# Performance work log

Measured on AMD Instinct MI355X. Metric: run time of the kernel, lower is better.

The kernel has to match this reference:

```python
import jax, jax.numpy as jnp
import numpy as np

B, N, K, C = 8, 8192, 16, 64
POS_HID, MULT = 64, 4
BN_EPS = 1e-3  # keras BatchNormalization default


def _bn(x, gamma, beta):
    # inference-mode BN with init moving stats (mean=0, var=1)
    return gamma * x * (1.0 / np.sqrt(1.0 + BN_EPS)) + beta


def setup_inputs() -> dict:
    key = jax.random.key(0)
    ks = jax.random.split(key, 16)
    d = {
        "key": jax.random.normal(ks[0], (B, N, C), jnp.float32),
        "query": jax.random.normal(ks[1], (B, N, C), jnp.float32),
        "value": jax.random.normal(ks[2], (B, N, C), jnp.float32),
        "pos": jax.random.normal(ks[3], (B, N, 3), jnp.float32),
        "idx": jax.random.randint(ks[4], (B, N, K), 0, N, jnp.int32),
        # pos_conv1: 1x1 conv 3 -> POS_HID (glorot), + BN params
        "W1": jax.random.normal(ks[5], (3, POS_HID), jnp.float32) * np.sqrt(2.0 / (3 + POS_HID)),
        "b1": jnp.zeros((POS_HID,), jnp.float32),
        "g1": jnp.ones((POS_HID,), jnp.float32) + 0.1 * jax.random.normal(ks[6], (POS_HID,), jnp.float32),
        "bt1": 0.1 * jax.random.normal(ks[7], (POS_HID,), jnp.float32),
        # pos_conv2: POS_HID -> C, no activation
        "W2": jax.random.normal(ks[8], (POS_HID, C), jnp.float32) * np.sqrt(2.0 / (POS_HID + C)),
        "b2": jnp.zeros((C,), jnp.float32),
        # attn_mlp1: C -> MULT*C, BN + relu
        "W3": jax.random.normal(ks[9], (C, MULT * C), jnp.float32) * np.sqrt(2.0 / (C + MULT * C)),
        "b3": jnp.zeros((MULT * C,), jnp.float32),
        "g3": jnp.ones((MULT * C,), jnp.float32) + 0.1 * jax.random.normal(ks[10], (MULT * C,), jnp.float32),
        "bt3": 0.1 * jax.random.normal(ks[11], (MULT * C,), jnp.float32),
        # attn_mlp2: MULT*C -> C, no activation
        "W4": jax.random.normal(ks[12], (MULT * C, C), jnp.float32) * np.sqrt(2.0 / (MULT * C + C)),
        "b4": jnp.zeros((C,), jnp.float32),
    }
    return d


def reference(key, query, value, pos, idx, W1, b1, g1, bt1, W2, b2, W3, b3, g3, bt3, W4, b4):
    # per-batch KNN gather: key [B,N,C], idx [B,N,K] -> [B,N,K,C]
    gather = jax.vmap(lambda t, i: t[i])
    k_nb = gather(key, idx)                         # [B,N,K,C]
    qk_rel = query[:, :, None, :] - k_nb            # [B,N,K,C]
    pos_rel = pos[:, :, None, :] - gather(pos, idx)  # [B,N,K,3]

    # positional embedding MLP (1x1 convs)
    h = jax.nn.relu(_bn(pos_rel @ W1 + b1, g1, bt1))  # [B,N,K,POS_HID]
    pos_em = h @ W2 + b2                              # [B,N,K,C]

    # attention MLP (subtraction-based vector attention)
    a = jax.nn.relu(_bn((qk_rel + pos_em) @ W3 + b3, g3, bt3))  # [B,N,K,4C]
    a = (a @ W4 + b4) / jnp.sqrt(jnp.asarray(C, jnp.float32))   # [B,N,K,C]
    # tf.nn.softmax default axis=-1 -> softmax over CHANNEL axis (faithful to source)
    a = jax.nn.softmax(a, axis=-1)

    v = value[:, :, None, :] + pos_em               # [B,N,K,C]
    # einsum 'b c i j, b c i j -> b c j' on channels-last: sum over neighbor axis K
    agg = jnp.sum(a * v, axis=2)                    # [B,N,C]
    return agg
```

## Files before the change

### kernel.cpp

```cpp
#include <hip/hip_runtime.h>
#include <hip/hip_bf16.h>

typedef __bf16 bf16x8 __attribute__((ext_vector_type(8)));
typedef __bf16 bf16x4 __attribute__((ext_vector_type(4)));
typedef float  f32x4  __attribute__((ext_vector_type(4)));

#define MFMA16(A,B,C) __builtin_amdgcn_mfma_f32_16x16x32_bf16((A),(B),(C),0,0,0)

constexpr int NB = 8, NN = 8192, KK = 16;
constexpr int XS = 72;
constexpr size_t WS_NEEDED = 78848;


__global__ void prep_kernel(const float* __restrict__ W1, const float* __restrict__ b1,
                            const float* __restrict__ g1, const float* __restrict__ bt1,
                            const float* __restrict__ W2, const float* __restrict__ W3,
                            const float* __restrict__ b3, const float* __restrict__ g3,
                            const float* __restrict__ bt3, const float* __restrict__ W4,
                            unsigned char* __restrict__ ws)
{
    __bf16* w3f = (__bf16*)(ws);
    __bf16* w4f = (__bf16*)(ws + 32768);
    __bf16* w2f = (__bf16*)(ws + 65536);
    __bf16* w1f = (__bf16*)(ws + 73728);
    float*  c3f = (float*)(ws + 77824);

    const float inv = 1.0f / sqrtf(1.0f + 1e-3f);
    int t = blockIdx.x * 256 + threadIdx.x;

    if (t < 16384) {
        int i = t & 7, lane = (t >> 3) & 63, r = t >> 9;
        int ks = r & 1, nb = r >> 1;
        int p = ks * 32 + (lane >> 4) * 8 + i;
        int c = (p & 3) * 16 + (p >> 2);
        int n = nb * 16 + (lane & 15);
        w3f[t] = (__bf16)(W3[c * 256 + n] * (g3[n] * inv));
    } else if (t < 32768) {
        int u = t - 16384;
        int i = u & 7, lane = (u >> 3) & 63, r = u >> 9;
        int kb = r & 7, nb = r >> 3;
        int q = (kb & 1) * 32 + (lane >> 4) * 8 + i;
        int c = (kb >> 1) * 64 + (q & 3) * 16 + (q >> 2);
        int n = nb * 16 + (lane & 15);
        w4f[u] = (__bf16)(W4[c * 64 + n] * 0.125f);
    } else if (t < 36864) {
        int u = t - 32768;
        int i = u & 7, lane = (u >> 3) & 63, r = u >> 9;
        int ks = r & 1, nb = r >> 1;
        int p = ks * 32 + (lane >> 4) * 8 + i;
        int c = (p & 3) * 16 + (p >> 2);
        int n = nb * 16 + (lane & 15);
        w2f[u] = (__bf16)(W2[c * 64 + n]);
    } else if (t < 38912) {
        int u = t - 36864;
        int i = u & 7, lane = (u >> 3) & 63, nb = u >> 9;
        int kk = (lane >> 4) * 8 + i;
        int n = nb * 16 + (lane & 15);
        float v = 0.f;
        if (kk < 3)       v = W1[kk * 64 + n] * (g1[n] * inv);
        else if (kk == 3) v = b1[n] * (g1[n] * inv) + bt1[n];
        w1f[u] = (__bf16)v;
    } else if (t < 39168) {
        int n = t - 38912;
        c3f[n] = b3[n] * (g3[n] * inv) + bt3[n];
    }
}

__global__ __launch_bounds__(256, 2) void fused_kernel(
    const float* __restrict__ key, const float* __restrict__ query,
    const float* __restrict__ value, const float* __restrict__ pos,
    const int* __restrict__ idx, const float* __restrict__ b2,
    const float* __restrict__ b4, const unsigned char* __restrict__ ws,
    float* __restrict__ out)
{
    const __bf16* w3f = (const __bf16*)(ws);
    const __bf16* w4f = (const __bf16*)(ws + 32768);
    const __bf16* w2f = (const __bf16*)(ws + 65536);
    const __bf16* w1f = (const __bf16*)(ws + 73728);
    const float*  c3f = (const float*)(ws + 77824);

    const f32x4 ZERO4 = {0.f, 0.f, 0.f, 0.f};

    __shared__ __attribute__((aligned(16))) __bf16 sX [4][32 * XS];
    __shared__ __attribute__((aligned(16))) __bf16 sA1[4][32 * XS];
    __shared__ __attribute__((aligned(16))) float  sPR[4][32][4];
    __shared__ int sJ[4][32];

    const int wv   = threadIdx.x >> 6;
    const int lane = threadIdx.x & 63;
    const int lg   = lane >> 4;
    const int ln   = lane & 15;

    const int ptbase = blockIdx.x * 8 + wv * 2;
    const int b  = ptbase >> 13;
    const int n0 = ptbase & 8191;

    __bf16* X  = sX[wv];
    __bf16* A1 = sA1[wv];

    if (lane < 32) {
        int p = lane >> 4, k = lane & 15;
        int n = n0 + p;
        int j = idx[(b * NN + n) * KK + k];
        sJ[wv][lane] = j;
        int pb = (b * NN + n) * 3, jb = (b * NN + j) * 3;
        sPR[wv][lane][0] = pos[pb + 0] - pos[jb + 0];
        sPR[wv][lane][1] = pos[pb + 1] - pos[jb + 1];
        sPR[wv][lane][2] = pos[pb + 2] - pos[jb + 2];
        sPR[wv][lane][3] = 0.f;
    }
    bf16x8 af[2];
    #pragma unroll
    for (int rb = 0; rb < 2; ++rb) {
        bf16x8 a;
        #pragma unroll
        for (int i = 0; i < 8; ++i) a[i] = (__bf16)0.0f;
        if (lg == 0) {
            const float4 pr = *(const float4*)&sPR[wv][rb * 16 + ln][0];
            a[0] = (__bf16)pr.x; a[1] = (__bf16)pr.y; a[2] = (__bf16)pr.z;
            a[3] = (__bf16)1.0f;
        }
        af[rb] = a;
    }
    f32x4 pa[2][4];
    #pragma unroll
    for (int nb = 0; nb < 4; ++nb) {
        bf16x8 wf = *(const bf16x8*)(w1f + (size_t)(nb * 64 + lane) * 8);
        pa[0][nb] = MFMA16(af[0], wf, ZERO4);
        pa[1][nb] = MFMA16(af[1], wf, ZERO4);
    }
    #pragma unroll
    for (int rb = 0; rb < 2; ++rb)
        #pragma unroll
        for (int jj = 0; jj < 4; ++jj) {
            int row = rb * 16 + lg * 4 + jj;
            bf16x4 hv;
            #pragma unroll
            for (int nb = 0; nb < 4; ++nb) hv[nb] = (__bf16)fmaxf(pa[rb][nb][jj], 0.f);
            *(bf16x4*)&X[row * XS + ln * 4] = hv;
        }

    bf16x8 hf[2][2];
    #pragma unroll
    for (int rb = 0; rb < 2; ++rb)
        #pragma unroll
        for (int ks = 0; ks < 2; ++ks)
            hf[rb][ks] = *(const bf16x8*)&X[(rb * 16 + ln) * XS + ks * 32 + lg * 8];
    f32x4 pacc[2][4];
    #pragma unroll
    for (int rb = 0; rb < 2; ++rb)
        #pragma unroll
        for (int cb = 0; cb < 4; ++cb) pacc[rb][cb] = ZERO4;
    #pragma unroll
    for (int cb = 0; cb < 4; ++cb)
        #pragma unroll
        for (int ks = 0; ks < 2; ++ks) {
            bf16x8 wf = *(const bf16x8*)(w2f + (size_t)((cb * 2 + ks) * 64 + lane) * 8);
            pacc[0][cb] = MFMA16(hf[0][ks], wf, pacc[0][cb]);
            pacc[1][cb] = MFMA16(hf[1][ks], wf, pacc[1][cb]);
        }

    float posem[2][4][4];
    #pragma unroll
    for (int rb = 0; rb < 2; ++rb) {
        const int nrow = n0 + rb;
        float qv[4];
        #pragma unroll
        for (int cb = 0; cb < 4; ++cb) {
            qv[cb] = query[(b * NN + nrow) * 64 + cb * 16 + ln];
            float c2v = b2[cb * 16 + ln];
            #pragma unroll
            for (int jj = 0; jj < 4; ++jj)
                posem[rb][cb][jj] = pacc[rb][cb][jj] + c2v;
        }
        #pragma unroll
        for (int jj = 0; jj < 4; ++jj) {
            int row = rb * 16 + lg * 4 + jj;
            int jb = (b * NN + sJ[wv][row]) * 64;
            bf16x4 xv;
            #pragma unroll
            for (int cb = 0; cb < 4; ++cb)
                xv[cb] = (__bf16)(qv[cb] - key[jb + cb * 16 + ln] + posem[rb][cb][jj]);
            *(bf16x4*)&X[row * XS + ln * 4] = xv;
        }
    }

    bf16x8 xf[2][2];
    #pragma unroll
    for (int rb = 0; rb < 2; ++rb)
        #pragma unroll
        for (int ks = 0; ks < 2; ++ks)
            xf[rb][ks] = *(const bf16x8*)&X[(rb * 16 + ln) * XS + ks * 32 + lg * 8];
    f32x4 acc2[2][4];
    #pragma unroll
    for (int rb = 0; rb < 2; ++rb)
        #pragma unroll
        for (int nb = 0; nb < 4; ++nb) acc2[rb][nb] = ZERO4;

    for (int cc = 0; cc < 4; ++cc) {
        f32x4 g1a[2][4];
        #pragma unroll
        for (int rb = 0; rb < 2; ++rb)
            #pragma unroll
            for (int cb = 0; cb < 4; ++cb) g1a[rb][cb] = ZERO4;
        #pragma unroll
        for (int cb = 0; cb < 4; ++cb) {
            int nb = cc * 4 + cb;
            #pragma unroll
            for (int ks = 0; ks < 2; ++ks) {
                bf16x8 wf = *(const bf16x8*)(w3f + (size_t)((nb * 2 + ks) * 64 + lane) * 8);
                g1a[0][cb] = MFMA16(xf[0][ks], wf, g1a[0][cb]);
                g1a[1][cb] = MFMA16(xf[1][ks], wf, g1a[1][cb]);
            }
        }
        float c3v[4];
        #pragma unroll
        for (int cb = 0; cb < 4; ++cb) c3v[cb] = c3f[(cc * 4 + cb) * 16 + ln];
        #pragma unroll
        for (int rb = 0; rb < 2; ++rb)
            #pragma unroll
            for (int jj = 0; jj < 4; ++jj) {
                int row = rb * 16 + lg * 4 + jj;
                bf16x4 av;
                #pragma unroll
                for (int cb = 0; cb < 4; ++cb)
                    av[cb] = (__bf16)fmaxf(g1a[rb][cb][jj] + c3v[cb], 0.f);
                *(bf16x4*)&A1[row * XS + ln * 4] = av;
            }
        #pragma unroll
        for (int kb2 = 0; kb2 < 2; ++kb2) {
            bf16x8 a1f[2];
            #pragma unroll
            for (int rb = 0; rb < 2; ++rb)
                a1f[rb] = *(const bf16x8*)&A1[(rb * 16 + ln) * XS + kb2 * 32 + lg * 8];
            #pragma unroll
            for (int nb = 0; nb < 4; ++nb) {
                bf16x8 wf = *(const bf16x8*)(w4f + (size_t)((nb * 8 + cc * 2 + kb2) * 64 + lane) * 8);
                acc2[0][nb] = MFMA16(a1f[0], wf, acc2[0][nb]);
                acc2[1][nb] = MFMA16(a1f[1], wf, acc2[1][nb]);
            }
        }
    }

    float b4v[4];
    #pragma unroll
    for (int nb = 0; nb < 4; ++nb) b4v[nb] = b4[nb * 16 + ln] * 0.125f;
    #pragma unroll
    for (int rb = 0; rb < 2; ++rb) {
        const int nrow = n0 + rb;
        float vv[4];
        #pragma unroll
        for (int nb = 0; nb < 4; ++nb) vv[nb] = value[(b * NN + nrow) * 64 + nb * 16 + ln];

        float res[4] = {0.f, 0.f, 0.f, 0.f};
        #pragma unroll
        for (int jj = 0; jj < 4; ++jj) {
            float e0 = __expf(acc2[rb][0][jj] + b4v[0]);
            float e1 = __expf(acc2[rb][1][jj] + b4v[1]);
            float e2 = __expf(acc2[rb][2][jj] + b4v[2]);
            float e3 = __expf(acc2[rb][3][jj] + b4v[3]);
            float s = (e0 + e1) + (e2 + e3);
            #pragma unroll
            for (int d = 1; d < 16; d <<= 1) s += __shfl_xor(s, d, 64);
            float inv = 1.0f / s;
            res[0] = fmaf(e0 * inv, vv[0] + posem[rb][0][jj], res[0]);
            res[1] = fmaf(e1 * inv, vv[1] + posem[rb][1][jj], res[1]);
            res[2] = fmaf(e2 * inv, vv[2] + posem[rb][2][jj], res[2]);
            res[3] = fmaf(e3 * inv, vv[3] + posem[rb][3][jj], res[3]);
        }
        #pragma unroll
        for (int nb = 0; nb < 4; ++nb) {
            res[nb] += __shfl_xor(res[nb], 16, 64);
            res[nb] += __shfl_xor(res[nb], 32, 64);
        }
        float o = (lg == 0) ? res[0] : (lg == 1) ? res[1] : (lg == 2) ? res[2] : res[3];
        out[(b * NN + nrow) * 64 + lane] = o;
    }
}

extern "C" void kernel_launch(void* const* d_in, const int* in_sizes, int n_in,
                              void* d_out, int out_size, void* d_ws, size_t ws_size,
                              hipStream_t stream) {
    const float* key   = (const float*)d_in[0];
    const float* query = (const float*)d_in[1];
    const float* value = (const float*)d_in[2];
    const float* pos   = (const float*)d_in[3];
    const int*   idx   = (const int*)d_in[4];
    const float* W1    = (const float*)d_in[5];
    const float* b1    = (const float*)d_in[6];
    const float* g1    = (const float*)d_in[7];
    const float* bt1   = (const float*)d_in[8];
    const float* W2    = (const float*)d_in[9];
    const float* b2    = (const float*)d_in[10];
    const float* W3    = (const float*)d_in[11];
    const float* b3    = (const float*)d_in[12];
    const float* g3    = (const float*)d_in[13];
    const float* bt3   = (const float*)d_in[14];
    const float* W4    = (const float*)d_in[15];
    const float* b4    = (const float*)d_in[16];
    unsigned char* ws  = (unsigned char*)d_ws;
    float* out = (float*)d_out;

    if (ws_size < WS_NEEDED) return;

    hipLaunchKernelGGL(prep_kernel, dim3(153), dim3(256), 0, stream,
                       W1, b1, g1, bt1, W2, W3, b3, g3, bt3, W4, ws);
    hipLaunchKernelGGL(fused_kernel, dim3(8192), dim3(256), 0, stream,
                       key, query, value, pos, idx, b2, b4, ws, out);
}
```

Before: 262.0 us.

## Hoist global loads early and fold biases into MFMA accumulator init

Moves the query, value, bias and gathered key loads to the start of the kernel so their latency overlaps the positional MLP MFMAs. Neighbour indices and relative positions now stay in registers and are broadcast with shuffles instead of going through shared memory. The b2, c3 and b4 biases are preloaded into the MFMA accumulators, which removes the separate add passes. The cost is more live registers, which at launch bounds (256,2) could cause spills or lower occupancy.

```diff
diff --git a/kernel.cpp b/kernel.cpp
--- a/kernel.cpp
+++ b/kernel.cpp
@@ -83,8 +83,6 @@
 
     __shared__ __attribute__((aligned(16))) __bf16 sX [4][32 * XS];
     __shared__ __attribute__((aligned(16))) __bf16 sA1[4][32 * XS];
-    __shared__ __attribute__((aligned(16))) float  sPR[4][32][4];
-    __shared__ int sJ[4][32];
 
     const int wv   = threadIdx.x >> 6;
     const int lane = threadIdx.x & 63;
@@ -98,26 +96,55 @@
     __bf16* X  = sX[wv];
     __bf16* A1 = sA1[wv];
 
+    float qv[2][4], vvv[2][4], b4v[4];
+    #pragma unroll
+    for (int rb = 0; rb < 2; ++rb)
+        #pragma unroll
+        for (int cb = 0; cb < 4; ++cb) {
+            qv[rb][cb]  = query[(b * NN + n0 + rb) * 64 + cb * 16 + ln];
+            vvv[rb][cb] = value[(b * NN + n0 + rb) * 64 + cb * 16 + ln];
+        }
+    #pragma unroll
+    for (int nb = 0; nb < 4; ++nb) b4v[nb] = b4[nb * 16 + ln] * 0.125f;
+    float b2v[4];
+    #pragma unroll
+    for (int cb = 0; cb < 4; ++cb) b2v[cb] = b2[cb * 16 + ln];
+
+    int   jl = 0;
+    float prx = 0.f, pry = 0.f, prz = 0.f;
     if (lane < 32) {
         int p = lane >> 4, k = lane & 15;
         int n = n0 + p;
-        int j = idx[(b * NN + n) * KK + k];
-        sJ[wv][lane] = j;
-        int pb = (b * NN + n) * 3, jb = (b * NN + j) * 3;
-        sPR[wv][lane][0] = pos[pb + 0] - pos[jb + 0];
-        sPR[wv][lane][1] = pos[pb + 1] - pos[jb + 1];
-        sPR[wv][lane][2] = pos[pb + 2] - pos[jb + 2];
-        sPR[wv][lane][3] = 0.f;
-    }
+        jl = idx[(b * NN + n) * KK + k];
+        int pb = (b * NN + n) * 3, jb = (b * NN + jl) * 3;
+        prx = pos[pb + 0] - pos[jb + 0];
+        pry = pos[pb + 1] - pos[jb + 1];
+        prz = pos[pb + 2] - pos[jb + 2];
+    }
+
+    float kreg[2][4][4];
+    #pragma unroll
+    for (int rb = 0; rb < 2; ++rb)
+        #pragma unroll
+        for (int jj = 0; jj < 4; ++jj) {
+            int j = __shfl(jl, rb * 16 + lg * 4 + jj, 64);
+            int jb = (b * NN + j) * 64;
+            #pragma unroll
+            for (int cb = 0; cb < 4; ++cb)
+                kreg[rb][jj][cb] = key[jb + cb * 16 + ln];
+        }
+
     bf16x8 af[2];
     #pragma unroll
     for (int rb = 0; rb < 2; ++rb) {
+        float ax = __shfl(prx, rb * 16 + ln, 64);
+        float ay = __shfl(pry, rb * 16 + ln, 64);
+        float az = __shfl(prz, rb * 16 + ln, 64);
         bf16x8 a;
         #pragma unroll
         for (int i = 0; i < 8; ++i) a[i] = (__bf16)0.0f;
         if (lg == 0) {
-            const float4 pr = *(const float4*)&sPR[wv][rb * 16 + ln][0];
-            a[0] = (__bf16)pr.x; a[1] = (__bf16)pr.y; a[2] = (__bf16)pr.z;
+            a[0] = (__bf16)ax; a[1] = (__bf16)ay; a[2] = (__bf16)az;
             a[3] = (__bf16)1.0f;
         }
         af[rb] = a;
@@ -150,7 +177,10 @@
     #pragma unroll
     for (int rb = 0; rb < 2; ++rb)
         #pragma unroll
-        for (int cb = 0; cb < 4; ++cb) pacc[rb][cb] = ZERO4;
+        for (int cb = 0; cb < 4; ++cb) {
+            f32x4 c0 = {b2v[cb], b2v[cb], b2v[cb], b2v[cb]};
+            pacc[rb][cb] = c0;
+        }
     #pragma unroll
     for (int cb = 0; cb < 4; ++cb)
         #pragma unroll
@@ -160,30 +190,17 @@
             pacc[1][cb] = MFMA16(hf[1][ks], wf, pacc[1][cb]);
         }
 
-    float posem[2][4][4];
-    #pragma unroll
-    for (int rb = 0; rb < 2; ++rb) {
-        const int nrow = n0 + rb;
-        float qv[4];
-        #pragma unroll
-        for (int cb = 0; cb < 4; ++cb) {
-            qv[cb] = query[(b * NN + nrow) * 64 + cb * 16 + ln];
-            float c2v = b2[cb * 16 + ln];
-            #pragma unroll
-            for (int jj = 0; jj < 4; ++jj)
-                posem[rb][cb][jj] = pacc[rb][cb][jj] + c2v;
-        }
+    #pragma unroll
+    for (int rb = 0; rb < 2; ++rb)
         #pragma unroll
         for (int jj = 0; jj < 4; ++jj) {
             int row = rb * 16 + lg * 4 + jj;
-            int jb = (b * NN + sJ[wv][row]) * 64;
             bf16x4 xv;
             #pragma unroll
             for (int cb = 0; cb < 4; ++cb)
-                xv[cb] = (__bf16)(qv[cb] - key[jb + cb * 16 + ln] + posem[rb][cb][jj]);
+                xv[cb] = (__bf16)(qv[rb][cb] - kreg[rb][jj][cb] + pacc[rb][cb][jj]);
             *(bf16x4*)&X[row * XS + ln * 4] = xv;
         }
-    }
 
     bf16x8 xf[2][2];
     #pragma unroll
@@ -195,14 +212,20 @@
     #pragma unroll
     for (int rb = 0; rb < 2; ++rb)
         #pragma unroll
-        for (int nb = 0; nb < 4; ++nb) acc2[rb][nb] = ZERO4;
+        for (int nb = 0; nb < 4; ++nb) {
+            f32x4 c0 = {b4v[nb], b4v[nb], b4v[nb], b4v[nb]};
+            acc2[rb][nb] = c0;
+        }
 
     for (int cc = 0; cc < 4; ++cc) {
         f32x4 g1a[2][4];
         #pragma unroll
-        for (int rb = 0; rb < 2; ++rb)
-            #pragma unroll
-            for (int cb = 0; cb < 4; ++cb) g1a[rb][cb] = ZERO4;
+        for (int cb = 0; cb < 4; ++cb) {
+            float c3v = c3f[(cc * 4 + cb) * 16 + ln];
+            f32x4 c0 = {c3v, c3v, c3v, c3v};
+            g1a[0][cb] = c0;
+            g1a[1][cb] = c0;
+        }
         #pragma unroll
         for (int cb = 0; cb < 4; ++cb) {
             int nb = cc * 4 + cb;
@@ -213,9 +236,6 @@
                 g1a[1][cb] = MFMA16(xf[1][ks], wf, g1a[1][cb]);
             }
         }
-        float c3v[4];
-        #pragma unroll
-        for (int cb = 0; cb < 4; ++cb) c3v[cb] = c3f[(cc * 4 + cb) * 16 + ln];
         #pragma unroll
         for (int rb = 0; rb < 2; ++rb)
             #pragma unroll
@@ -224,7 +244,7 @@
                 bf16x4 av;
                 #pragma unroll
                 for (int cb = 0; cb < 4; ++cb)
-                    av[cb] = (__bf16)fmaxf(g1a[rb][cb][jj] + c3v[cb], 0.f);
+                    av[cb] = (__bf16)fmaxf(g1a[rb][cb][jj], 0.f);
                 *(bf16x4*)&A1[row * XS + ln * 4] = av;
             }
         #pragma unroll
@@ -242,31 +262,24 @@
         }
     }
 
-    float b4v[4];
-    #pragma unroll
-    for (int nb = 0; nb < 4; ++nb) b4v[nb] = b4[nb * 16 + ln] * 0.125f;
     #pragma unroll
     for (int rb = 0; rb < 2; ++rb) {
         const int nrow = n0 + rb;
-        float vv[4];
-        #pragma unroll
-        for (int nb = 0; nb < 4; ++nb) vv[nb] = value[(b * NN + nrow) * 64 + nb * 16 + ln];
-
         float res[4] = {0.f, 0.f, 0.f, 0.f};
         #pragma unroll
         for (int jj = 0; jj < 4; ++jj) {
-            float e0 = __expf(acc2[rb][0][jj] + b4v[0]);
-            float e1 = __expf(acc2[rb][1][jj] + b4v[1]);
-            float e2 = __expf(acc2[rb][2][jj] + b4v[2]);
-            float e3 = __expf(acc2[rb][3][jj] + b4v[3]);
+            float e0 = __expf(acc2[rb][0][jj]);
+            float e1 = __expf(acc2[rb][1][jj]);
+            float e2 = __expf(acc2[rb][2][jj]);
+            float e3 = __expf(acc2[rb][3][jj]);
             float s = (e0 + e1) + (e2 + e3);
             #pragma unroll
             for (int d = 1; d < 16; d <<= 1) s += __shfl_xor(s, d, 64);
             float inv = 1.0f / s;
-            res[0] = fmaf(e0 * inv, vv[0] + posem[rb][0][jj], res[0]);
-            res[1] = fmaf(e1 * inv, vv[1] + posem[rb][1][jj], res[1]);
-            res[2] = fmaf(e2 * inv, vv[2] + posem[rb][2][jj], res[2]);
-            res[3] = fmaf(e3 * inv, vv[3] + posem[rb][3][jj], res[3]);
+            res[0] = fmaf(e0 * inv, vvv[rb][0] + pacc[rb][0][jj], res[0]);
+            res[1] = fmaf(e1 * inv, vvv[rb][1] + pacc[rb][1][jj], res[1]);
+            res[2] = fmaf(e2 * inv, vvv[rb][2] + pacc[rb][2][jj], res[2]);
+            res[3] = fmaf(e3 * inv, vvv[rb][3] + pacc[rb][3][jj], res[3]);
         }
         #pragma unroll
         for (int nb = 0; nb < 4; ++nb) {
```

Result: no change. 257.2 us (-1.8%).
